# Kernel tuning notes

Hardware: AMD Instinct MI355X
Metric: run time of the kernel (lower is better)

## Reference

```python
import jax, jax.numpy as jnp
import numpy as np
import math

D_MODEL = 1024
N_HEADS = 16
HEAD_DIM = 64
BATCH = 2
SEQ = 2048


def setup_inputs() -> dict:
    key = jax.random.key(0)
    ks = jax.random.split(key, 5)
    x = jax.random.normal(ks[0], (BATCH, SEQ, D_MODEL), dtype=jnp.float32)
    s = 0.02
    wq = jax.random.normal(ks[1], (D_MODEL, D_MODEL), dtype=jnp.float32) * s
    wk = jax.random.normal(ks[2], (D_MODEL, D_MODEL), dtype=jnp.float32) * s
    wv = jax.random.normal(ks[3], (D_MODEL, D_MODEL), dtype=jnp.float32) * s
    wo = jax.random.normal(ks[4], (D_MODEL, D_MODEL), dtype=jnp.float32) * s
    gammas = jnp.linspace(0.9, 0.99, N_HEADS, dtype=jnp.float32)
    return {"x": x, "wq": wq, "wk": wk, "wv": wv, "wo": wo, "gammas": gammas}


def _decay_mask(length: int, gammas: jnp.ndarray, dtype) -> jnp.ndarray:
    # [H, L, L]: gamma^(t-s) for t >= s, else 0 (causal exponential decay)
    pos = jnp.arange(length)
    diff = pos[:, None] - pos[None, :]
    causal = diff >= 0
    d = jnp.maximum(diff, 0).astype(dtype)
    g = gammas.astype(dtype)[:, None, None]
    return jnp.where(causal[None], jnp.power(g, d[None]), jnp.zeros((), dtype))


def reference(x, wq, wk, wv, wo, gammas):
    B, L, D = x.shape
    H, hd = N_HEADS, HEAD_DIM
    # torch nn.Linear: y = x @ W.T
    q = (x @ wq.T).reshape(B, L, H, hd)
    k = (x @ wk.T).reshape(B, L, H, hd)
    v = (x @ wv.T).reshape(B, L, H, hd)
    scale = 1.0 / math.sqrt(hd)
    scores = jnp.einsum('bthd,bshd->bhts', q * scale, k)  # [B,H,L,L]
    decay = _decay_mask(L, gammas, x.dtype)               # [H,L,L]
    weights = scores * decay[None]
    retained = jnp.einsum('bhts,bshd->bthd', weights, v)  # [B,L,H,hd]
    return retained.reshape(B, L, H * hd) @ wo.T
```

## Files before the change

kernel.cpp:

```cpp
#include <hip/hip_runtime.h>


typedef __attribute__((ext_vector_type(8))) short bf16x8;
typedef __attribute__((ext_vector_type(4))) float f32x4;
typedef __attribute__((ext_vector_type(16))) float f32x16;
typedef __attribute__((ext_vector_type(4))) unsigned short u16x4;
typedef __attribute__((ext_vector_type(8))) unsigned short u16x8;
typedef __attribute__((ext_vector_type(4))) unsigned int u32x4;

__device__ inline unsigned short f2bf(float f) {
    unsigned int u;
    __builtin_memcpy(&u, &f, 4);
    u += 0x7fffu + ((u >> 16) & 1u);
    return (unsigned short)(u >> 16);
}
__device__ inline float bf2f(unsigned short us) {
    unsigned int u = (unsigned int)us << 16;
    float f;
    __builtin_memcpy(&f, &u, 4);
    return f;
}

__device__ inline f32x4 mfma16(bf16x8 a, bf16x8 b, f32x4 c) {
    return __builtin_amdgcn_mfma_f32_16x16x32_bf16(a, b, c, 0, 0, 0);
}
__device__ inline f32x16 mfma32(bf16x8 a, bf16x8 b, f32x16 c) {
    return __builtin_amdgcn_mfma_f32_32x32x16_bf16(a, b, c, 0, 0, 0);
}

__device__ inline void gl16(const unsigned short* g, unsigned short* l) {
    __builtin_amdgcn_global_load_lds(
        (const __attribute__((address_space(1))) unsigned int*)g,
        (__attribute__((address_space(3))) unsigned int*)l,
        16, 0, 0);
}

__device__ inline unsigned cvtpk(float lo, float hi) {
    unsigned r;
    asm("v_cvt_pk_bf16_f32 %0, %1, %2" : "=v"(r) : "v"(lo), "v"(hi));
    return r;
}

__global__ __launch_bounds__(256) void convert_bf16(
    const float* __restrict__ x,
    const float* __restrict__ wq, const float* __restrict__ wk,
    const float* __restrict__ wv, const float* __restrict__ wo,
    unsigned short* __restrict__ xb,
    unsigned short* __restrict__ wqb, unsigned short* __restrict__ wkb,
    unsigned short* __restrict__ wvb, unsigned short* __restrict__ wob)
{
    int cid = blockIdx.x * 256 + threadIdx.x;
    #pragma unroll
    for (int it = 0; it < 4; ++it, cid += 262144) {
        const float* src;
        unsigned short* dst;
        size_t off;
        if (cid < 524288) {
            src = x; dst = xb; off = (size_t)cid * 8;
        } else {
            const int t = cid - 524288;
            const int seg = t >> 17;
            off = (size_t)(t & 131071) * 8;
            src = seg == 0 ? wq : seg == 1 ? wk : seg == 2 ? wv : wo;
            dst = seg == 0 ? wqb : seg == 1 ? wkb : seg == 2 ? wvb : wob;
        }
        f32x4 a = *(const f32x4*)(src + off);
        f32x4 b = *(const f32x4*)(src + off + 4);
        u32x4 v = { cvtpk(a[0], a[1]), cvtpk(a[2], a[3]),
                    cvtpk(b[0], b[1]), cvtpk(b[2], b[3]) };
        *(u32x4*)(dst + off) = v;
    }
}

__global__ __launch_bounds__(256) void qkv_bf16(
    const unsigned short* __restrict__ xb,
    const unsigned short* __restrict__ wqb, const unsigned short* __restrict__ wkb,
    const unsigned short* __restrict__ wvb,
    unsigned short* __restrict__ qfr, unsigned short* __restrict__ kfr,
    unsigned short* __restrict__ vfr)
{
    __shared__ unsigned short sR[128 * 64];
    __shared__ unsigned short sL[128 * 64];

    const int z = blockIdx.z;
    const unsigned short* W = (z == 0) ? wqb : (z == 1) ? wkb : wvb;
    const unsigned short* Rs = (z < 2) ? xb : W;
    const unsigned short* Ls = (z < 2) ? W : xb;
    const int rblk = (z < 2) ? blockIdx.x : blockIdx.y;
    const int lblk = (z < 2) ? blockIdx.y : blockIdx.x;

    const int tid = threadIdx.x;
    const int l = tid & 63, w = tid >> 6;
    const int lrow = l & 15, koff4 = (l >> 4) * 4;
    const int swz = lrow & 7;
    const int wrow = (w >> 1) * 64, wcol = (w & 1) * 64;

    f32x4 acc[4][4] = {};

    const int srow = w * 32 + (l >> 3);
    const int scol = ((l & 7) ^ ((l >> 3) & 7)) * 8;
    const unsigned short* gR = Rs + (size_t)(rblk * 128 + srow) * 1024 + scol;
    const unsigned short* gL = Ls + (size_t)(lblk * 128 + srow) * 1024 + scol;
    unsigned short* lRb = sR + (w * 32) * 64;
    unsigned short* lLb = sL + (w * 32) * 64;

    auto stage = [&](int kk) {
        #pragma unroll
        for (int p = 0; p < 4; ++p) {
            gl16(gR + (size_t)p * 8 * 1024 + kk, lRb + p * 512);
            gl16(gL + (size_t)p * 8 * 1024 + kk, lLb + p * 512);
        }
    };

    stage(0);
    for (int kk = 0; kk < 1024; kk += 64) {
        asm volatile("s_waitcnt vmcnt(0)" ::: "memory");
        __builtin_amdgcn_s_barrier();
        __builtin_amdgcn_sched_barrier(0);

        bf16x8 aL[2][4], bR[2][4];
        #pragma unroll
        for (int kt = 0; kt < 2; ++kt)
            #pragma unroll
            for (int f = 0; f < 4; ++f) {
                const int co = ((kt * 4 + (l >> 4)) ^ swz) * 8;
                aL[kt][f] = *(const bf16x8*)&sL[(wcol + f * 16 + lrow) * 64 + co];
                bR[kt][f] = *(const bf16x8*)&sR[(wrow + f * 16 + lrow) * 64 + co];
            }
        asm volatile("s_waitcnt lgkmcnt(0)" ::: "memory");
        __builtin_amdgcn_sched_barrier(0);
        __builtin_amdgcn_s_barrier();
        __builtin_amdgcn_sched_barrier(0);

        if (kk + 64 < 1024) stage(kk + 64);

        __builtin_amdgcn_s_setprio(1);
        #pragma unroll
        for (int kt = 0; kt < 2; ++kt)
            #pragma unroll
            for (int af = 0; af < 4; ++af)
                #pragma unroll
                for (int bf = 0; bf < 4; ++bf)
                    acc[af][bf] = mfma16(aL[kt][af], bR[kt][bf], acc[af][bf]);
        __builtin_amdgcn_s_setprio(0);
    }

    #pragma unroll
    for (int af = 0; af < 4; ++af) {
        #pragma unroll
        for (int bf = 0; bf < 4; ++bf) {
            const int m = rblk * 128 + wrow + bf * 16 + lrow;
            const int n0 = lblk * 128 + wcol + af * 16 + koff4;
            f32x4 v = acc[af][bf];
            unsigned p0 = cvtpk(v[0], v[1]), p1 = cvtpk(v[2], v[3]);
            u16x4 val = { (unsigned short)(p0 & 0xffff), (unsigned short)(p0 >> 16),
                          (unsigned short)(p1 & 0xffff), (unsigned short)(p1 >> 16) };
            if (z < 2) {
                const int bq = m >> 11, s = m & 2047;
                const int h2 = n0 >> 6, dd = n0 & 63;
                const size_t addr = (size_t)((bq * 16 + h2) * 64 + (s >> 5)) * 2048
                                  + (size_t)(dd >> 4) * 512 + (size_t)((dd >> 3) & 1) * 256
                                  + (size_t)(s & 31) * 8 + (dd & 7);
                unsigned short* dst = z ? kfr : qfr;
                *(u16x4*)(dst + addr) = val;
            } else {
                const int h2 = m >> 6, dd = m & 63;
                const int bq = n0 >> 11, t = n0 & 2047;
                const size_t addr = (size_t)((bq * 16 + h2) * 64 + (t >> 5)) * 2048
                                  + (size_t)((dd >> 5) * 2 + ((t >> 4) & 1)) * 512
                                  + (size_t)((t >> 3) & 1) * 256
                                  + (size_t)(dd & 31) * 8 + (t & 7);
                *(u16x4*)(vfr + addr) = val;
            }
        }
    }
}

__global__ __launch_bounds__(128) void a_state(
    const unsigned short* __restrict__ kfr, const unsigned short* __restrict__ vfr,
    const float* __restrict__ gammas, unsigned short* __restrict__ states)
{
    __shared__ unsigned short kbuf[4096];

    const int bid = blockIdx.x;
    const int bh = bid & 31, c = bid >> 5;
    const int b = bh >> 4, h = bh & 15;
    const float lg = log2f(gammas[h]);
    const float gi1 = exp2f(-lg);

    const int tid = threadIdx.x;
    const int l = tid & 63, w = tid >> 6;
    const int l31 = l & 31, hi = l >> 5;

    const size_t hbase = (size_t)((b * 16 + h) * 64) * 2048;
    const unsigned short* src = kfr + hbase + (size_t)c * 4096;
    #pragma unroll
    for (int p = 0; p < 4; ++p)
        gl16(src + (w * 4 + p) * 512 + l * 8, kbuf + (w * 4 + p) * 512 + l * 8);
    asm volatile("s_waitcnt vmcnt(0)" ::: "memory");
    __builtin_amdgcn_s_barrier();
    __builtin_amdgcn_sched_barrier(0);

    const unsigned short* vfb = vfr + hbase + l * 8;
    const int dd = 32 * w + l31;
    const int dbase = (dd >> 4) * 512 + ((dd >> 3) & 1) * 256 + (dd & 7);

    f32x16 as0 = {}, as1 = {};
    #pragma unroll
    for (int sl = 0; sl < 2; ++sl) {
        bf16x8 vc[4];
        #pragma unroll
        for (int i = 0; i < 4; ++i)
            vc[i] = *(const bf16x8*)(vfb + (size_t)(2 * c + sl) * 2048 + i * 512);
        bf16x8 kt[2];
        #pragma unroll
        for (int kti = 0; kti < 2; ++kti) {
            float fac = exp2f(lg * (float)(64 - (32 * sl + 16 * kti + 8 * hi)));
            unsigned pk[4];
            #pragma unroll
            for (int jj = 0; jj < 4; ++jj) {
                const int s0 = 16 * kti + 8 * hi + 2 * jj;
                float e0 = bf2f(kbuf[sl * 2048 + dbase + s0 * 8]) * fac;
                fac *= gi1;
                float e1 = bf2f(kbuf[sl * 2048 + dbase + (s0 + 1) * 8]) * fac;
                fac *= gi1;
                pk[jj] = cvtpk(e0, e1);
            }
            u32x4 kv_ = { pk[0], pk[1], pk[2], pk[3] };
            kt[kti] = __builtin_bit_cast(bf16x8, kv_);
        }
        as0 = mfma32(kt[0], vc[0], as0);
        as0 = mfma32(kt[1], vc[1], as0);
        as1 = mfma32(kt[0], vc[2], as1);
        as1 = mfma32(kt[1], vc[3], as1);
    }

    unsigned short* sbase = states + (size_t)(bh * 32 + c) * 4096;
    #pragma unroll
    for (int r = 0; r < 16; ++r) {
        const int crow = (r & 3) + (hi << 2) + ((r >> 2) << 3);
        const size_t a = (size_t)(2 * w + (crow >> 4)) * 1024
                       + (size_t)((crow >> 3) & 1) * 256 + (crow & 7) + (size_t)l31 * 8;
        sbase[a]       = f2bf(as0[r]);
        sbase[a + 512] = f2bf(as1[r]);
    }
}

__global__ __launch_bounds__(256) void state_scan(
    unsigned short* __restrict__ states, const float* __restrict__ gammas)
{
    const int bh = blockIdx.x;
    const float g64 = exp2f(64.0f * log2f(gammas[bh & 15]));
    unsigned short* base = states + (size_t)bh * 32 * 4096 + threadIdx.x * 16;

    float S[16] = {};
    u16x8 a0 = *(const u16x8*)(base);
    u16x8 a1 = *(const u16x8*)(base + 8);
    for (int c = 0; c < 32; ++c) {
        u16x8 n0, n1;
        if (c + 1 < 32) {
            n0 = *(const u16x8*)(base + (size_t)(c + 1) * 4096);
            n1 = *(const u16x8*)(base + (size_t)(c + 1) * 4096 + 8);
        }
        u16x8 o0, o1;
        #pragma unroll
        for (int e = 0; e < 8; ++e) {
            S[e] = S[e] * g64 + bf2f(a0[e]);
            o0[e] = f2bf(S[e]);
        }
        #pragma unroll
        for (int e = 0; e < 8; ++e) {
            S[8 + e] = S[8 + e] * g64 + bf2f(a1[e]);
            o1[e] = f2bf(S[8 + e]);
        }
        *(u16x8*)(base + (size_t)c * 4096) = o0;
        *(u16x8*)(base + (size_t)c * 4096 + 8) = o1;
        a0 = n0; a1 = n1;
    }
}

__global__ __launch_bounds__(128) void chunk_out(
    const unsigned short* __restrict__ qfr, const unsigned short* __restrict__ kfr,
    const unsigned short* __restrict__ vfr, const unsigned short* __restrict__ states,
    const float* __restrict__ gammas, unsigned short* __restrict__ ret)
{
    const int bid = blockIdx.x;
    const int bh = bid & 31, c = bid >> 5;
    const int b = bh >> 4, h = bh & 15;
    const float lg = log2f(gammas[h]);

    const int tid = threadIdx.x;
    const int l = tid & 63, w = tid >> 6;
    const int l31 = l & 31, hi = l >> 5;
    const int gt = 2 * c + w;

    const size_t hbase = (size_t)((b * 16 + h) * 64) * 2048;
    const unsigned short* qfb = qfr + hbase + l * 8;
    const unsigned short* kfb = kfr + hbase + l * 8;
    const unsigned short* vfb = vfr + hbase + l * 8;

    bf16x8 qf[4];
    #pragma unroll
    for (int kt = 0; kt < 4; ++kt)
        qf[kt] = *(const bf16x8*)(qfb + (size_t)gt * 2048 + kt * 512);

    f32x16 acc0 = {}, acc1 = {};

    if (c > 0) {
        const unsigned short* sb_ = states + (size_t)(bh * 32 + c - 1) * 4096 + l * 8;
        bf16x8 sf[4][2];
        #pragma unroll
        for (int kt = 0; kt < 4; ++kt)
            #pragma unroll
            for (int dh = 0; dh < 2; ++dh)
                sf[kt][dh] = *(const bf16x8*)(sb_ + kt * 1024 + dh * 512);
        f32x16 a0 = {}, a1 = {};
        #pragma unroll
        for (int kt = 0; kt < 4; ++kt) {
            a0 = mfma32(qf[kt], sf[kt][0], a0);
            a1 = mfma32(qf[kt], sf[kt][1], a1);
        }
        #pragma unroll
        for (int r = 0; r < 16; ++r) {
            const int crow = (r & 3) + (hi << 2) + ((r >> 2) << 3);
            const float sfac = 0.125f * exp2f(lg * (float)(32 * w + crow));
            acc0[r] = a0[r] * sfac;
            acc1[r] = a1[r] * sfac;
        }
    }

    float cf[16];
    #pragma unroll
    for (int r = 0; r < 16; ++r) {
        const int crow = (r & 3) + (hi << 2) + ((r >> 2) << 3);
        cf[r] = exp2f((float)(31 - crow) * lg);
    }
    for (int sl = 0; sl <= w; ++sl) {
        const int gs = 2 * c + sl;
        bf16x8 kc[4], vc[4];
        #pragma unroll
        for (int kt = 0; kt < 4; ++kt)
            kc[kt] = *(const bf16x8*)(kfb + (size_t)gs * 2048 + kt * 512);
        #pragma unroll
        for (int i = 0; i < 4; ++i)
            vc[i] = *(const bf16x8*)(vfb + (size_t)gs * 2048 + i * 512);

        f32x16 sc = {};
        #pragma unroll
        for (int kt = 0; kt < 4; ++kt) sc = mfma32(kc[kt], qf[kt], sc);

        const float rowf = 0.125f * exp2f((float)((w - sl) * 32 + l31 - 31) * lg);
        float wv_[16];
        if (sl == w) {
            #pragma unroll
            for (int r = 0; r < 16; ++r) {
                const int crow = (r & 3) + (hi << 2) + ((r >> 2) << 3);
                float t_ = sc[r] * rowf * cf[r];
                wv_[r] = (l31 >= crow) ? t_ : 0.0f;
            }
        } else {
            #pragma unroll
            for (int r = 0; r < 16; ++r) wv_[r] = sc[r] * rowf * cf[r];
        }
        unsigned pk_[8];
        #pragma unroll
        for (int i = 0; i < 8; ++i) pk_[i] = cvtpk(wv_[2 * i], wv_[2 * i + 1]);
        asm("v_permlane32_swap_b32 %0, %1" : "+v"(pk_[0]), "+v"(pk_[2]));
        asm("v_permlane32_swap_b32 %0, %1" : "+v"(pk_[1]), "+v"(pk_[3]));
        asm("v_permlane32_swap_b32 %0, %1" : "+v"(pk_[4]), "+v"(pk_[6]));
        asm("v_permlane32_swap_b32 %0, %1" : "+v"(pk_[5]), "+v"(pk_[7]));
        u32x4 f0v = { pk_[0], pk_[1], pk_[2], pk_[3] };
        u32x4 f1v = { pk_[4], pk_[5], pk_[6], pk_[7] };
        const bf16x8 pa0 = __builtin_bit_cast(bf16x8, f0v);
        const bf16x8 pa1 = __builtin_bit_cast(bf16x8, f1v);
        acc0 = mfma32(pa0, vc[0], acc0);
        acc0 = mfma32(pa1, vc[1], acc0);
        acc1 = mfma32(pa0, vc[2], acc1);
        acc1 = mfma32(pa1, vc[3], acc1);
    }

    #pragma unroll
    for (int r = 0; r < 16; ++r) {
        const int tl = (r & 3) + (hi << 2) + ((r >> 2) << 3);
        unsigned short* dst = ret + (size_t)(b * 2048 + gt * 32 + tl) * 1024 + h * 64 + l31;
        dst[0]  = f2bf(acc0[r]);
        dst[32] = f2bf(acc1[r]);
    }
}

__global__ __launch_bounds__(256) void out_bf16(
    const unsigned short* __restrict__ ret, const unsigned short* __restrict__ wob,
    float* __restrict__ out)
{
    __shared__ unsigned short sR[128 * 64];
    __shared__ unsigned short sL[128 * 64];

    const int rblk = blockIdx.x;
    const int lblk = blockIdx.y;

    const int tid = threadIdx.x;
    const int l = tid & 63, w = tid >> 6;
    const int lrow = l & 15, koff4 = (l >> 4) * 4;
    const int swz = lrow & 7;
    const int wrow = (w >> 1) * 64, wcol = (w & 1) * 64;

    f32x4 acc[4][4] = {};

    const int srow = w * 32 + (l >> 3);
    const int scol = ((l & 7) ^ ((l >> 3) & 7)) * 8;
    const unsigned short* gR = ret + (size_t)(rblk * 128 + srow) * 1024 + scol;
    const unsigned short* gL = wob + (size_t)(lblk * 128 + srow) * 1024 + scol;
    unsigned short* lRb = sR + (w * 32) * 64;
    unsigned short* lLb = sL + (w * 32) * 64;

    auto stage = [&](int kk) {
        #pragma unroll
        for (int p = 0; p < 4; ++p) {
            gl16(gR + (size_t)p * 8 * 1024 + kk, lRb + p * 512);
            gl16(gL + (size_t)p * 8 * 1024 + kk, lLb + p * 512);
        }
    };

    stage(0);
    for (int kk = 0; kk < 1024; kk += 64) {
        asm volatile("s_waitcnt vmcnt(0)" ::: "memory");
        __builtin_amdgcn_s_barrier();
        __builtin_amdgcn_sched_barrier(0);

        bf16x8 aL[2][4], bR[2][4];
        #pragma unroll
        for (int kt = 0; kt < 2; ++kt)
            #pragma unroll
            for (int f = 0; f < 4; ++f) {
                const int co = ((kt * 4 + (l >> 4)) ^ swz) * 8;
                aL[kt][f] = *(const bf16x8*)&sL[(wcol + f * 16 + lrow) * 64 + co];
                bR[kt][f] = *(const bf16x8*)&sR[(wrow + f * 16 + lrow) * 64 + co];
            }
        asm volatile("s_waitcnt lgkmcnt(0)" ::: "memory");
        __builtin_amdgcn_sched_barrier(0);
        __builtin_amdgcn_s_barrier();
        __builtin_amdgcn_sched_barrier(0);

        if (kk + 64 < 1024) stage(kk + 64);

        __builtin_amdgcn_s_setprio(1);
        #pragma unroll
        for (int kt = 0; kt < 2; ++kt)
            #pragma unroll
            for (int af = 0; af < 4; ++af)
                #pragma unroll
                for (int bf = 0; bf < 4; ++bf)
                    acc[af][bf] = mfma16(aL[kt][af], bR[kt][bf], acc[af][bf]);
        __builtin_amdgcn_s_setprio(0);
    }

    #pragma unroll
    for (int af = 0; af < 4; ++af)
        #pragma unroll
        for (int bf = 0; bf < 4; ++bf) {
            const int m = rblk * 128 + wrow + bf * 16 + lrow;
            const int n0 = lblk * 128 + wcol + af * 16 + koff4;
            *(f32x4*)(out + (size_t)m * 1024 + n0) = acc[af][bf];
        }
}

extern "C" void kernel_launch(void* const* d_in, const int* in_sizes, int n_in,
                              void* d_out, int out_size, void* d_ws, size_t ws_size,
                              hipStream_t stream) {
    const float* x      = (const float*)d_in[0];
    const float* wq     = (const float*)d_in[1];
    const float* wk     = (const float*)d_in[2];
    const float* wv     = (const float*)d_in[3];
    const float* wo     = (const float*)d_in[4];
    const float* gammas = (const float*)d_in[5];
    float* out = (float*)d_out;

    unsigned short* ws = (unsigned short*)d_ws;
    const size_t M = 1024 * 1024;
    unsigned short* qf     = ws;
    unsigned short* kf     = ws + 4 * M;
    unsigned short* vf     = ws + 8 * M;
    unsigned short* ret    = ws + 12 * M;
    unsigned short* xb     = ret;
    unsigned short* wqb    = ws + 16 * M;
    unsigned short* wkb    = ws + 17 * M;
    unsigned short* wvb    = ws + 18 * M;
    unsigned short* states = ws + 16 * M;
    unsigned short* wob    = ws + 20 * M;

    convert_bf16<<<1024, 256, 0, stream>>>(x, wq, wk, wv, wo, xb, wqb, wkb, wvb, wob);
    qkv_bf16<<<dim3(32, 8, 3), 256, 0, stream>>>(xb, wqb, wkb, wvb, qf, kf, vf);
    a_state<<<1024, 128, 0, stream>>>(kf, vf, gammas, states);
    state_scan<<<32, 256, 0, stream>>>(states, gammas);
    chunk_out<<<1024, 128, 0, stream>>>(qf, kf, vf, states, gammas, ret);
    out_bf16<<<dim3(32, 8), 256, 0, stream>>>(ret, wob, out);
}
```

Measured before the change: 86.14 us.

## Fuse Q and K projections into one block sharing the staged x tile

```diff
diff --git a/kernel.cpp b/kernel.cpp
--- a/kernel.cpp
+++ b/kernel.cpp
@@ -72,98 +72,187 @@
     }
 }
 
-__global__ __launch_bounds__(256) void qkv_bf16(
+__global__ __launch_bounds__(256) void qkv2_bf16(
     const unsigned short* __restrict__ xb,
     const unsigned short* __restrict__ wqb, const unsigned short* __restrict__ wkb,
     const unsigned short* __restrict__ wvb,
     unsigned short* __restrict__ qfr, unsigned short* __restrict__ kfr,
     unsigned short* __restrict__ vfr)
 {
-    __shared__ unsigned short sR[128 * 64];
-    __shared__ unsigned short sL[128 * 64];
+    __shared__ unsigned short sX[128 * 64];
+    __shared__ unsigned short sQ[128 * 64];
+    __shared__ unsigned short sK[128 * 64];
 
     const int z = blockIdx.z;
-    const unsigned short* W = (z == 0) ? wqb : (z == 1) ? wkb : wvb;
-    const unsigned short* Rs = (z < 2) ? xb : W;
-    const unsigned short* Ls = (z < 2) ? W : xb;
-    const int rblk = (z < 2) ? blockIdx.x : blockIdx.y;
-    const int lblk = (z < 2) ? blockIdx.y : blockIdx.x;
-
     const int tid = threadIdx.x;
     const int l = tid & 63, w = tid >> 6;
     const int lrow = l & 15, koff4 = (l >> 4) * 4;
     const int swz = lrow & 7;
     const int wrow = (w >> 1) * 64, wcol = (w & 1) * 64;
 
-    f32x4 acc[4][4] = {};
-
     const int srow = w * 32 + (l >> 3);
     const int scol = ((l & 7) ^ ((l >> 3) & 7)) * 8;
-    const unsigned short* gR = Rs + (size_t)(rblk * 128 + srow) * 1024 + scol;
-    const unsigned short* gL = Ls + (size_t)(lblk * 128 + srow) * 1024 + scol;
-    unsigned short* lRb = sR + (w * 32) * 64;
-    unsigned short* lLb = sL + (w * 32) * 64;
-
-    auto stage = [&](int kk) {
-        #pragma unroll
-        for (int p = 0; p < 4; ++p) {
-            gl16(gR + (size_t)p * 8 * 1024 + kk, lRb + p * 512);
-            gl16(gL + (size_t)p * 8 * 1024 + kk, lLb + p * 512);
-        }
-    };
-
-    stage(0);
-    for (int kk = 0; kk < 1024; kk += 64) {
-        asm volatile("s_waitcnt vmcnt(0)" ::: "memory");
-        __builtin_amdgcn_s_barrier();
-        __builtin_amdgcn_sched_barrier(0);
-
-        bf16x8 aL[2][4], bR[2][4];
-        #pragma unroll
-        for (int kt = 0; kt < 2; ++kt)
+
+    if (z == 0) {
+        const int rblk = blockIdx.x;
+        const int lblk = blockIdx.y;
+
+        const unsigned short* gX = xb  + (size_t)(rblk * 128 + srow) * 1024 + scol;
+        const unsigned short* gQ = wqb + (size_t)(lblk * 128 + srow) * 1024 + scol;
+        const unsigned short* gK = wkb + (size_t)(lblk * 128 + srow) * 1024 + scol;
+        unsigned short* lX = sX + (w * 32) * 64;
+        unsigned short* lQ = sQ + (w * 32) * 64;
+        unsigned short* lK = sK + (w * 32) * 64;
+
+        auto stage = [&](int kk) {
+            #pragma unroll
+            for (int p = 0; p < 4; ++p) {
+                gl16(gX + (size_t)p * 8 * 1024 + kk, lX + p * 512);
+                gl16(gQ + (size_t)p * 8 * 1024 + kk, lQ + p * 512);
+                gl16(gK + (size_t)p * 8 * 1024 + kk, lK + p * 512);
+            }
+        };
+
+        f32x4 accq[4][4] = {}, acck[4][4] = {};
+
+        stage(0);
+        for (int kk = 0; kk < 1024; kk += 64) {
+            asm volatile("s_waitcnt vmcnt(0)" ::: "memory");
+            __builtin_amdgcn_s_barrier();
+            __builtin_amdgcn_sched_barrier(0);
+
+            bf16x8 a0q[4], a0k[4], b0[4];
             #pragma unroll
             for (int f = 0; f < 4; ++f) {
-                const int co = ((kt * 4 + (l >> 4)) ^ swz) * 8;
-                aL[kt][f] = *(const bf16x8*)&sL[(wcol + f * 16 + lrow) * 64 + co];
-                bR[kt][f] = *(const bf16x8*)&sR[(wrow + f * 16 + lrow) * 64 + co];
-            }
-        asm volatile("s_waitcnt lgkmcnt(0)" ::: "memory");
-        __builtin_amdgcn_sched_barrier(0);
-        __builtin_amdgcn_s_barrier();
-        __builtin_amdgcn_sched_barrier(0);
-
-        if (kk + 64 < 1024) stage(kk + 64);
-
-        __builtin_amdgcn_s_setprio(1);
-        #pragma unroll
-        for (int kt = 0; kt < 2; ++kt)
+                const int co = ((0 * 4 + (l >> 4)) ^ swz) * 8;
+                a0q[f] = *(const bf16x8*)&sQ[(wcol + f * 16 + lrow) * 64 + co];
+                a0k[f] = *(const bf16x8*)&sK[(wcol + f * 16 + lrow) * 64 + co];
+                b0[f]  = *(const bf16x8*)&sX[(wrow + f * 16 + lrow) * 64 + co];
+            }
+            __builtin_amdgcn_s_setprio(1);
             #pragma unroll
             for (int af = 0; af < 4; ++af)
                 #pragma unroll
-                for (int bf = 0; bf < 4; ++bf)
-                    acc[af][bf] = mfma16(aL[kt][af], bR[kt][bf], acc[af][bf]);
-        __builtin_amdgcn_s_setprio(0);
-    }
-
-    #pragma unroll
-    for (int af = 0; af < 4; ++af) {
-        #pragma unroll
-        for (int bf = 0; bf < 4; ++bf) {
-            const int m = rblk * 128 + wrow + bf * 16 + lrow;
-            const int n0 = lblk * 128 + wcol + af * 16 + koff4;
-            f32x4 v = acc[af][bf];
-            unsigned p0 = cvtpk(v[0], v[1]), p1 = cvtpk(v[2], v[3]);
-            u16x4 val = { (unsigned short)(p0 & 0xffff), (unsigned short)(p0 >> 16),
-                          (unsigned short)(p1 & 0xffff), (unsigned short)(p1 >> 16) };
-            if (z < 2) {
+                for (int bf = 0; bf < 4; ++bf) {
+                    accq[af][bf] = mfma16(a0q[af], b0[bf], accq[af][bf]);
+                    acck[af][bf] = mfma16(a0k[af], b0[bf], acck[af][bf]);
+                }
+            __builtin_amdgcn_s_setprio(0);
+            bf16x8 a1q[4], a1k[4], b1[4];
+            #pragma unroll
+            for (int f = 0; f < 4; ++f) {
+                const int co = ((1 * 4 + (l >> 4)) ^ swz) * 8;
+                a1q[f] = *(const bf16x8*)&sQ[(wcol + f * 16 + lrow) * 64 + co];
+                a1k[f] = *(const bf16x8*)&sK[(wcol + f * 16 + lrow) * 64 + co];
+                b1[f]  = *(const bf16x8*)&sX[(wrow + f * 16 + lrow) * 64 + co];
+            }
+            asm volatile("s_waitcnt lgkmcnt(0)" ::: "memory");
+            __builtin_amdgcn_sched_barrier(0);
+            __builtin_amdgcn_s_barrier();
+            __builtin_amdgcn_sched_barrier(0);
+
+            if (kk + 64 < 1024) stage(kk + 64);
+
+            __builtin_amdgcn_s_setprio(1);
+            #pragma unroll
+            for (int af = 0; af < 4; ++af)
+                #pragma unroll
+                for (int bf = 0; bf < 4; ++bf) {
+                    accq[af][bf] = mfma16(a1q[af], b1[bf], accq[af][bf]);
+                    acck[af][bf] = mfma16(a1k[af], b1[bf], acck[af][bf]);
+                }
+            __builtin_amdgcn_s_setprio(0);
+        }
+
+        #pragma unroll
+        for (int af = 0; af < 4; ++af) {
+            #pragma unroll
+            for (int bf = 0; bf < 4; ++bf) {
+                const int m = rblk * 128 + wrow + bf * 16 + lrow;
+                const int n0 = lblk * 128 + wcol + af * 16 + koff4;
                 const int bq = m >> 11, s = m & 2047;
                 const int h2 = n0 >> 6, dd = n0 & 63;
                 const size_t addr = (size_t)((bq * 16 + h2) * 64 + (s >> 5)) * 2048
                                   + (size_t)(dd >> 4) * 512 + (size_t)((dd >> 3) & 1) * 256
                                   + (size_t)(s & 31) * 8 + (dd & 7);
-                unsigned short* dst = z ? kfr : qfr;
-                *(u16x4*)(dst + addr) = val;
-            } else {
+                {
+                    f32x4 v = accq[af][bf];
+                    unsigned p0 = cvtpk(v[0], v[1]), p1 = cvtpk(v[2], v[3]);
+                    u16x4 val = { (unsigned short)(p0 & 0xffff), (unsigned short)(p0 >> 16),
+                                  (unsigned short)(p1 & 0xffff), (unsigned short)(p1 >> 16) };
+                    *(u16x4*)(qfr + addr) = val;
+                }
+                {
+                    f32x4 v = acck[af][bf];
+                    unsigned p0 = cvtpk(v[0], v[1]), p1 = cvtpk(v[2], v[3]);
+                    u16x4 val = { (unsigned short)(p0 & 0xffff), (unsigned short)(p0 >> 16),
+                                  (unsigned short)(p1 & 0xffff), (unsigned short)(p1 >> 16) };
+                    *(u16x4*)(kfr + addr) = val;
+                }
+            }
+        }
+    } else {
+        const int rblk = blockIdx.y;
+        const int lblk = blockIdx.x;
+
+        const unsigned short* gR = wvb + (size_t)(rblk * 128 + srow) * 1024 + scol;
+        const unsigned short* gL = xb  + (size_t)(lblk * 128 + srow) * 1024 + scol;
+        unsigned short* lRb = sX + (w * 32) * 64;
+        unsigned short* lLb = sQ + (w * 32) * 64;
+
+        auto stage = [&](int kk) {
+            #pragma unroll
+            for (int p = 0; p < 4; ++p) {
+                gl16(gR + (size_t)p * 8 * 1024 + kk, lRb + p * 512);
+                gl16(gL + (size_t)p * 8 * 1024 + kk, lLb + p * 512);
+            }
+        };
+
+        f32x4 acc[4][4] = {};
+
+        stage(0);
+        for (int kk = 0; kk < 1024; kk += 64) {
+            asm volatile("s_waitcnt vmcnt(0)" ::: "memory");
+            __builtin_amdgcn_s_barrier();
+            __builtin_amdgcn_sched_barrier(0);
+
+            bf16x8 aL[2][4], bR[2][4];
+            #pragma unroll
+            for (int kt = 0; kt < 2; ++kt)
+                #pragma unroll
+                for (int f = 0; f < 4; ++f) {
+                    const int co = ((kt * 4 + (l >> 4)) ^ swz) * 8;
+                    aL[kt][f] = *(const bf16x8*)&sQ[(wcol + f * 16 + lrow) * 64 + co];
+                    bR[kt][f] = *(const bf16x8*)&sX[(wrow + f * 16 + lrow) * 64 + co];
+                }
+            asm volatile("s_waitcnt lgkmcnt(0)" ::: "memory");
+            __builtin_amdgcn_sched_barrier(0);
+            __builtin_amdgcn_s_barrier();
+            __builtin_amdgcn_sched_barrier(0);
+
+            if (kk + 64 < 1024) stage(kk + 64);
+
+            __builtin_amdgcn_s_setprio(1);
+            #pragma unroll
+            for (int kt = 0; kt < 2; ++kt)
+                #pragma unroll
+                for (int af = 0; af < 4; ++af)
+                    #pragma unroll
+                    for (int bf = 0; bf < 4; ++bf)
+                        acc[af][bf] = mfma16(aL[kt][af], bR[kt][bf], acc[af][bf]);
+            __builtin_amdgcn_s_setprio(0);
+        }
+
+        #pragma unroll
+        for (int af = 0; af < 4; ++af)
+            #pragma unroll
+            for (int bf = 0; bf < 4; ++bf) {
+                const int m = rblk * 128 + wrow + bf * 16 + lrow;
+                const int n0 = lblk * 128 + wcol + af * 16 + koff4;
+                f32x4 v = acc[af][bf];
+                unsigned p0 = cvtpk(v[0], v[1]), p1 = cvtpk(v[2], v[3]);
+                u16x4 val = { (unsigned short)(p0 & 0xffff), (unsigned short)(p0 >> 16),
+                              (unsigned short)(p1 & 0xffff), (unsigned short)(p1 >> 16) };
                 const int h2 = m >> 6, dd = m & 63;
                 const int bq = n0 >> 11, t = n0 & 2047;
                 const size_t addr = (size_t)((bq * 16 + h2) * 64 + (t >> 5)) * 2048
@@ -172,7 +261,6 @@
                                   + (size_t)(dd & 31) * 8 + (t & 7);
                 *(u16x4*)(vfr + addr) = val;
             }
-        }
     }
 }
 
@@ -489,7 +577,7 @@
     unsigned short* wob    = ws + 20 * M;
 
     convert_bf16<<<1024, 256, 0, stream>>>(x, wq, wk, wv, wo, xb, wqb, wkb, wvb, wob);
-    qkv_bf16<<<dim3(32, 8, 3), 256, 0, stream>>>(xb, wqb, wkb, wvb, qf, kf, vf);
+    qkv2_bf16<<<dim3(32, 8, 2), 256, 0, stream>>>(xb, wqb, wkb, wvb, qf, kf, vf);
     a_state<<<1024, 128, 0, stream>>>(kf, vf, gammas, states);
     state_scan<<<32, 256, 0, stream>>>(states, gammas);
     chunk_out<<<1024, 128, 0, stream>>>(qf, kf, vf, states, gammas, ret);
```

Result: slower. 101.3 us (+17.6%).

## Double-buffer LDS tiles in QKV and output GEMMs to deepen prefetch

Applied to the files above, without the earlier changes.

```diff
diff --git a/kernel.cpp b/kernel.cpp
--- a/kernel.cpp
+++ b/kernel.cpp
@@ -79,8 +79,10 @@
     unsigned short* __restrict__ qfr, unsigned short* __restrict__ kfr,
     unsigned short* __restrict__ vfr)
 {
-    __shared__ unsigned short sR[128 * 64];
-    __shared__ unsigned short sL[128 * 64];
+    __shared__ unsigned short sR0[128 * 64];
+    __shared__ unsigned short sR1[128 * 64];
+    __shared__ unsigned short sL0[128 * 64];
+    __shared__ unsigned short sL1[128 * 64];
 
     const int z = blockIdx.z;
     const unsigned short* W = (z == 0) ? wqb : (z == 1) ? wkb : wvb;
@@ -101,20 +103,25 @@
     const int scol = ((l & 7) ^ ((l >> 3) & 7)) * 8;
     const unsigned short* gR = Rs + (size_t)(rblk * 128 + srow) * 1024 + scol;
     const unsigned short* gL = Ls + (size_t)(lblk * 128 + srow) * 1024 + scol;
-    unsigned short* lRb = sR + (w * 32) * 64;
-    unsigned short* lLb = sL + (w * 32) * 64;
-
-    auto stage = [&](int kk) {
+    unsigned short* lR0 = sR0 + (w * 32) * 64;
+    unsigned short* lR1 = sR1 + (w * 32) * 64;
+    unsigned short* lL0 = sL0 + (w * 32) * 64;
+    unsigned short* lL1 = sL1 + (w * 32) * 64;
+
+    auto stageTo = [&](int kk, unsigned short* lR, unsigned short* lL) {
         #pragma unroll
         for (int p = 0; p < 4; ++p) {
-            gl16(gR + (size_t)p * 8 * 1024 + kk, lRb + p * 512);
-            gl16(gL + (size_t)p * 8 * 1024 + kk, lLb + p * 512);
+            gl16(gR + (size_t)p * 8 * 1024 + kk, lR + p * 512);
+            gl16(gL + (size_t)p * 8 * 1024 + kk, lL + p * 512);
         }
     };
 
-    stage(0);
-    for (int kk = 0; kk < 1024; kk += 64) {
-        asm volatile("s_waitcnt vmcnt(0)" ::: "memory");
+    auto body = [&](const unsigned short* sRb, const unsigned short* sLb,
+                    unsigned short* lR, unsigned short* lL,
+                    int kstage, bool cnt8) {
+        if (cnt8) asm volatile("s_waitcnt vmcnt(8)" ::: "memory");
+        else      asm volatile("s_waitcnt vmcnt(0)" ::: "memory");
+        __builtin_amdgcn_sched_barrier(0);
         __builtin_amdgcn_s_barrier();
         __builtin_amdgcn_sched_barrier(0);
 
@@ -124,15 +131,15 @@
             #pragma unroll
             for (int f = 0; f < 4; ++f) {
                 const int co = ((kt * 4 + (l >> 4)) ^ swz) * 8;
-                aL[kt][f] = *(const bf16x8*)&sL[(wcol + f * 16 + lrow) * 64 + co];
-                bR[kt][f] = *(const bf16x8*)&sR[(wrow + f * 16 + lrow) * 64 + co];
+                aL[kt][f] = *(const bf16x8*)&sLb[(wcol + f * 16 + lrow) * 64 + co];
+                bR[kt][f] = *(const bf16x8*)&sRb[(wrow + f * 16 + lrow) * 64 + co];
             }
         asm volatile("s_waitcnt lgkmcnt(0)" ::: "memory");
         __builtin_amdgcn_sched_barrier(0);
         __builtin_amdgcn_s_barrier();
         __builtin_amdgcn_sched_barrier(0);
 
-        if (kk + 64 < 1024) stage(kk + 64);
+        if (kstage < 1024) stageTo(kstage, lR, lL);
 
         __builtin_amdgcn_s_setprio(1);
         #pragma unroll
@@ -143,6 +150,13 @@
                 for (int bf = 0; bf < 4; ++bf)
                     acc[af][bf] = mfma16(aL[kt][af], bR[kt][bf], acc[af][bf]);
         __builtin_amdgcn_s_setprio(0);
+    };
+
+    stageTo(0, lR0, lL0);
+    stageTo(64, lR1, lL1);
+    for (int kb = 0; kb < 1024; kb += 128) {
+        body(sR0, sL0, lR0, lL0, kb + 128, true);
+        body(sR1, sL1, lR1, lL1, kb + 192, (kb + 128) < 1024);
     }
 
     #pragma unroll
@@ -392,8 +406,10 @@
     const unsigned short* __restrict__ ret, const unsigned short* __restrict__ wob,
     float* __restrict__ out)
 {
-    __shared__ unsigned short sR[128 * 64];
-    __shared__ unsigned short sL[128 * 64];
+    __shared__ unsigned short sR0[128 * 64];
+    __shared__ unsigned short sR1[128 * 64];
+    __shared__ unsigned short sL0[128 * 64];
+    __shared__ unsigned short sL1[128 * 64];
 
     const int rblk = blockIdx.x;
     const int lblk = blockIdx.y;
@@ -410,20 +426,25 @@
     const int scol = ((l & 7) ^ ((l >> 3) & 7)) * 8;
     const unsigned short* gR = ret + (size_t)(rblk * 128 + srow) * 1024 + scol;
     const unsigned short* gL = wob + (size_t)(lblk * 128 + srow) * 1024 + scol;
-    unsigned short* lRb = sR + (w * 32) * 64;
-    unsigned short* lLb = sL + (w * 32) * 64;
-
-    auto stage = [&](int kk) {
+    unsigned short* lR0 = sR0 + (w * 32) * 64;
+    unsigned short* lR1 = sR1 + (w * 32) * 64;
+    unsigned short* lL0 = sL0 + (w * 32) * 64;
+    unsigned short* lL1 = sL1 + (w * 32) * 64;
+
+    auto stageTo = [&](int kk, unsigned short* lR, unsigned short* lL) {
         #pragma unroll
         for (int p = 0; p < 4; ++p) {
-            gl16(gR + (size_t)p * 8 * 1024 + kk, lRb + p * 512);
-            gl16(gL + (size_t)p * 8 * 1024 + kk, lLb + p * 512);
+            gl16(gR + (size_t)p * 8 * 1024 + kk, lR + p * 512);
+            gl16(gL + (size_t)p * 8 * 1024 + kk, lL + p * 512);
         }
     };
 
-    stage(0);
-    for (int kk = 0; kk < 1024; kk += 64) {
-        asm volatile("s_waitcnt vmcnt(0)" ::: "memory");
+    auto body = [&](const unsigned short* sRb, const unsigned short* sLb,
+                    unsigned short* lR, unsigned short* lL,
+                    int kstage, bool cnt8) {
+        if (cnt8) asm volatile("s_waitcnt vmcnt(8)" ::: "memory");
+        else      asm volatile("s_waitcnt vmcnt(0)" ::: "memory");
+        __builtin_amdgcn_sched_barrier(0);
         __builtin_amdgcn_s_barrier();
         __builtin_amdgcn_sched_barrier(0);
 
@@ -433,15 +454,15 @@
             #pragma unroll
             for (int f = 0; f < 4; ++f) {
                 const int co = ((kt * 4 + (l >> 4)) ^ swz) * 8;
-                aL[kt][f] = *(const bf16x8*)&sL[(wcol + f * 16 + lrow) * 64 + co];
-                bR[kt][f] = *(const bf16x8*)&sR[(wrow + f * 16 + lrow) * 64 + co];
+                aL[kt][f] = *(const bf16x8*)&sLb[(wcol + f * 16 + lrow) * 64 + co];
+                bR[kt][f] = *(const bf16x8*)&sRb[(wrow + f * 16 + lrow) * 64 + co];
             }
         asm volatile("s_waitcnt lgkmcnt(0)" ::: "memory");
         __builtin_amdgcn_sched_barrier(0);
         __builtin_amdgcn_s_barrier();
         __builtin_amdgcn_sched_barrier(0);
 
-        if (kk + 64 < 1024) stage(kk + 64);
+        if (kstage < 1024) stageTo(kstage, lR, lL);
 
         __builtin_amdgcn_s_setprio(1);
         #pragma unroll
@@ -452,6 +473,13 @@
                 for (int bf = 0; bf < 4; ++bf)
                     acc[af][bf] = mfma16(aL[kt][af], bR[kt][bf], acc[af][bf]);
         __builtin_amdgcn_s_setprio(0);
+    };
+
+    stageTo(0, lR0, lL0);
+    stageTo(64, lR1, lL1);
+    for (int kb = 0; kb < 1024; kb += 128) {
+        body(sR0, sL0, lR0, lL0, kb + 128, true);
+        body(sR1, sL1, lR1, lL1, kb + 192, (kb + 128) < 1024);
     }
 
     #pragma unroll
```

Measured after the change: 86.97 us. Within noise of the previous version (+1.0%).

## Enlarge QKV GEMM tile to 256x256 with 8 waves and split-K LDS/MFMA interleave

Applied to the files above, without the earlier changes.

```diff
diff --git a/kernel.cpp b/kernel.cpp
--- a/kernel.cpp
+++ b/kernel.cpp
@@ -72,35 +72,39 @@
     }
 }
 
-__global__ __launch_bounds__(256) void qkv_bf16(
+__global__ __launch_bounds__(512) void qkv_bf16(
     const unsigned short* __restrict__ xb,
     const unsigned short* __restrict__ wqb, const unsigned short* __restrict__ wkb,
     const unsigned short* __restrict__ wvb,
     unsigned short* __restrict__ qfr, unsigned short* __restrict__ kfr,
     unsigned short* __restrict__ vfr)
 {
-    __shared__ unsigned short sR[128 * 64];
-    __shared__ unsigned short sL[128 * 64];
+    __shared__ unsigned short sR[256 * 64];
+    __shared__ unsigned short sL[256 * 64];
 
     const int z = blockIdx.z;
+    const int gx = blockIdx.x;
+    const int gy = blockIdx.y;
     const unsigned short* W = (z == 0) ? wqb : (z == 1) ? wkb : wvb;
     const unsigned short* Rs = (z < 2) ? xb : W;
     const unsigned short* Ls = (z < 2) ? W : xb;
-    const int rblk = (z < 2) ? blockIdx.x : blockIdx.y;
-    const int lblk = (z < 2) ? blockIdx.y : blockIdx.x;
+    const int rblk = (z < 2) ? gx : gy;
+    const int lblk = (z < 2) ? gy : gx;
 
     const int tid = threadIdx.x;
     const int l = tid & 63, w = tid >> 6;
     const int lrow = l & 15, koff4 = (l >> 4) * 4;
     const int swz = lrow & 7;
-    const int wrow = (w >> 1) * 64, wcol = (w & 1) * 64;
-
-    f32x4 acc[4][4] = {};
+    const int wm = w >> 2, wn = w & 3;
+    const int lbase = wm * 128;
+    const int rbase = wn * 64;
+
+    f32x4 acc[8][4] = {};
 
     const int srow = w * 32 + (l >> 3);
     const int scol = ((l & 7) ^ ((l >> 3) & 7)) * 8;
-    const unsigned short* gR = Rs + (size_t)(rblk * 128 + srow) * 1024 + scol;
-    const unsigned short* gL = Ls + (size_t)(lblk * 128 + srow) * 1024 + scol;
+    const unsigned short* gR = Rs + (size_t)(rblk * 256 + srow) * 1024 + scol;
+    const unsigned short* gL = Ls + (size_t)(lblk * 256 + srow) * 1024 + scol;
     unsigned short* lRb = sR + (w * 32) * 64;
     unsigned short* lLb = sL + (w * 32) * 64;
 
@@ -115,20 +119,42 @@
     stage(0);
     for (int kk = 0; kk < 1024; kk += 64) {
         asm volatile("s_waitcnt vmcnt(0)" ::: "memory");
+        __builtin_amdgcn_sched_barrier(0);
         __builtin_amdgcn_s_barrier();
         __builtin_amdgcn_sched_barrier(0);
 
-        bf16x8 aL[2][4], bR[2][4];
-        #pragma unroll
-        for (int kt = 0; kt < 2; ++kt)
-            #pragma unroll
-            for (int f = 0; f < 4; ++f) {
-                const int co = ((kt * 4 + (l >> 4)) ^ swz) * 8;
-                aL[kt][f] = *(const bf16x8*)&sL[(wcol + f * 16 + lrow) * 64 + co];
-                bR[kt][f] = *(const bf16x8*)&sR[(wrow + f * 16 + lrow) * 64 + co];
-            }
+        bf16x8 a0[8], b0[4];
+        {
+            const int co = ((l >> 4) ^ swz) * 8;
+            #pragma unroll
+            for (int f = 0; f < 8; ++f)
+                a0[f] = *(const bf16x8*)&sL[(lbase + f * 16 + lrow) * 64 + co];
+            #pragma unroll
+            for (int f = 0; f < 4; ++f)
+                b0[f] = *(const bf16x8*)&sR[(rbase + f * 16 + lrow) * 64 + co];
+        }
         asm volatile("s_waitcnt lgkmcnt(0)" ::: "memory");
         __builtin_amdgcn_sched_barrier(0);
+        __builtin_amdgcn_s_setprio(1);
+        #pragma unroll
+        for (int af = 0; af < 8; ++af)
+            #pragma unroll
+            for (int bf = 0; bf < 4; ++bf)
+                acc[af][bf] = mfma16(a0[af], b0[bf], acc[af][bf]);
+        __builtin_amdgcn_s_setprio(0);
+
+        bf16x8 a1[8], b1[4];
+        {
+            const int co = ((4 + (l >> 4)) ^ swz) * 8;
+            #pragma unroll
+            for (int f = 0; f < 8; ++f)
+                a1[f] = *(const bf16x8*)&sL[(lbase + f * 16 + lrow) * 64 + co];
+            #pragma unroll
+            for (int f = 0; f < 4; ++f)
+                b1[f] = *(const bf16x8*)&sR[(rbase + f * 16 + lrow) * 64 + co];
+        }
+        asm volatile("s_waitcnt lgkmcnt(0)" ::: "memory");
+        __builtin_amdgcn_sched_barrier(0);
         __builtin_amdgcn_s_barrier();
         __builtin_amdgcn_sched_barrier(0);
 
@@ -136,21 +162,19 @@
 
         __builtin_amdgcn_s_setprio(1);
         #pragma unroll
-        for (int kt = 0; kt < 2; ++kt)
-            #pragma unroll
-            for (int af = 0; af < 4; ++af)
-                #pragma unroll
-                for (int bf = 0; bf < 4; ++bf)
-                    acc[af][bf] = mfma16(aL[kt][af], bR[kt][bf], acc[af][bf]);
+        for (int af = 0; af < 8; ++af)
+            #pragma unroll
+            for (int bf = 0; bf < 4; ++bf)
+                acc[af][bf] = mfma16(a1[af], b1[bf], acc[af][bf]);
         __builtin_amdgcn_s_setprio(0);
     }
 
     #pragma unroll
-    for (int af = 0; af < 4; ++af) {
+    for (int af = 0; af < 8; ++af) {
         #pragma unroll
         for (int bf = 0; bf < 4; ++bf) {
-            const int m = rblk * 128 + wrow + bf * 16 + lrow;
-            const int n0 = lblk * 128 + wcol + af * 16 + koff4;
+            const int m = rblk * 256 + rbase + bf * 16 + lrow;
+            const int n0 = lblk * 256 + lbase + af * 16 + koff4;
             f32x4 v = acc[af][bf];
             unsigned p0 = cvtpk(v[0], v[1]), p1 = cvtpk(v[2], v[3]);
             u16x4 val = { (unsigned short)(p0 & 0xffff), (unsigned short)(p0 >> 16),
@@ -489,7 +513,7 @@
     unsigned short* wob    = ws + 20 * M;
 
     convert_bf16<<<1024, 256, 0, stream>>>(x, wq, wk, wv, wo, xb, wqb, wkb, wvb, wob);
-    qkv_bf16<<<dim3(32, 8, 3), 256, 0, stream>>>(xb, wqb, wkb, wvb, qf, kf, vf);
+    qkv_bf16<<<dim3(16, 4, 3), 512, 0, stream>>>(xb, wqb, wkb, wvb, qf, kf, vf);
     a_state<<<1024, 128, 0, stream>>>(kf, vf, gammas, states);
     state_scan<<<32, 256, 0, stream>>>(states, gammas);
     chunk_out<<<1024, 128, 0, stream>>>(qf, kf, vf, states, gammas, ret);
```

Result: slower. 91.49 us (+6.2%).
